# Kernel tuning notes

Measured on AMD Instinct MI355X. Metric: run time of the kernel, lower is better.

Reference implementation:

```python
import jax, jax.numpy as jnp
import numpy as np

K = 3
PAD = 1


def _conv_offset(x, w_off, b_off):
    # standard 3x3 conv, stride 1, pad 1, with bias -> [B, 18, H, W]
    y = jax.lax.conv_general_dilated(
        x, w_off, window_strides=(1, 1), padding=((PAD, PAD), (PAD, PAD)),
        dimension_numbers=('NCHW', 'OIHW', 'NCHW'))
    return y + b_off[None, :, None, None]


def _deform_conv(x, offset, w_dcn):
    # x: [B,Cin,H,W], offset: [B,2*K*K,H,W] (dy,dx interleaved per tap), w_dcn: [Cout,Cin,K,K]
    B, Cin, H, W = x.shape
    KK = K * K
    Ho, Wo = offset.shape[2], offset.shape[3]

    ky = jnp.repeat(jnp.arange(K), K)          # [KK] kernel row index
    kx = jnp.tile(jnp.arange(K), K)            # [KK] kernel col index
    off = offset.reshape(B, KK, 2, Ho, Wo)
    dy, dx = off[:, :, 0], off[:, :, 1]        # [B,KK,Ho,Wo]

    gy = (jnp.arange(Ho)[None, :, None] - PAD + ky[:, None, None]).astype(x.dtype)  # [KK,Ho,1]
    gx = (jnp.arange(Wo)[None, None, :] - PAD + kx[:, None, None]).astype(x.dtype)  # [KK,1,Wo]
    py = gy[None] + dy                         # [B,KK,Ho,Wo] sampling rows
    px = gx[None] + dx                         # [B,KK,Ho,Wo] sampling cols

    y0 = jnp.floor(py); x0 = jnp.floor(px)
    wy1 = py - y0; wx1 = px - x0
    wy0 = 1.0 - wy1; wx0 = 1.0 - wx1

    x_flat = x.reshape(B, Cin, H * W)

    def gather(yi, xi, wgt):
        valid = (yi >= 0) & (yi <= H - 1) & (xi >= 0) & (xi <= W - 1)
        yc = jnp.clip(yi, 0, H - 1).astype(jnp.int32)
        xc = jnp.clip(xi, 0, W - 1).astype(jnp.int32)
        idx = yc * W + xc                      # [B,KK,Ho,Wo]
        vals = jax.vmap(lambda xb, ib: xb[:, ib])(x_flat, idx)  # [B,Cin,KK,Ho,Wo]
        w = (wgt * valid.astype(x.dtype))[:, None]              # [B,1,KK,Ho,Wo]
        return vals * w

    sampled = (gather(y0, x0, wy0 * wx0)
               + gather(y0, x0 + 1, wy0 * wx1)
               + gather(y0 + 1, x0, wy1 * wx0)
               + gather(y0 + 1, x0 + 1, wy1 * wx1))  # [B,Cin,KK,Ho,Wo]

    wr = w_dcn.reshape(w_dcn.shape[0], Cin, KK)
    return jnp.einsum('bckhw,ock->bohw', sampled, wr)


def setup_inputs() -> dict:
    key = jax.random.key(0)
    k1, k2, k3, k4 = jax.random.split(key, 4)
    B, Cin, H, W = 8, 32, 160, 160
    Cout = 32
    x = jax.random.normal(k1, (B, Cin, H, W), jnp.float32)
    w_off = jax.random.normal(k2, (2 * K * K, Cin, K, K), jnp.float32) * 0.01
    b_off = jax.random.normal(k3, (2 * K * K,), jnp.float32) * 0.01
    w_dcn = jax.random.normal(k4, (Cout, Cin, K, K), jnp.float32) * 0.1
    return {'x': x, 'w_off': w_off, 'b_off': b_off, 'w_dcn': w_dcn}


def reference(x, w_off, b_off, w_dcn):
    offset = _conv_offset(x, w_off, b_off)
    y = _deform_conv(x, offset, w_dcn)
    return jax.nn.relu(y)
```

## Files before the change

### kernel.cpp

```cpp
#include <hip/hip_runtime.h>

#define H_ 160
#define W_ 160
#define HW_ (H_ * W_)
#define NPIX (8 * HW_)


typedef __attribute__((ext_vector_type(8)))  short  short8;
typedef __attribute__((ext_vector_type(4)))  float  f32x4;
typedef __attribute__((ext_vector_type(2)))  float  f32x2;
typedef __attribute__((ext_vector_type(16))) float  f32x16;
typedef __attribute__((ext_vector_type(4)))  unsigned u32x4;

__device__ __forceinline__ unsigned short bf16_rne(float f) {
    unsigned u = __float_as_uint(f);
    u += 0x7fffu + ((u >> 16) & 1u);
    return (unsigned short)(u >> 16);
}
__device__ __forceinline__ unsigned pack2_bf16(float a, float b) {
    unsigned ua = __float_as_uint(a); ua += 0x7fffu + ((ua >> 16) & 1u);
    unsigned ub = __float_as_uint(b); ub += 0x7fffu + ((ub >> 16) & 1u);
    return (ua >> 16) | (ub & 0xffff0000u);
}
__device__ __forceinline__ f32x2 up2(unsigned u) {
    f32x2 r;
    r.x = __uint_as_float(u << 16);
    r.y = __uint_as_float(u & 0xffff0000u);
    return r;
}

__global__ __launch_bounds__(256) void nhwc_bf16(
    const float* __restrict__ x, unsigned short* __restrict__ xT)
{
    const int pix = blockIdx.x * 256 + threadIdx.x;
    const int p = pix % HW_;
    const int b = pix / HW_;
    const float* __restrict__ src = x + (size_t)b * 32 * HW_ + p;
    unsigned* __restrict__ dst = (unsigned*)(xT + (size_t)pix * 32);
    #pragma unroll
    for (int g = 0; g < 16; ++g)
        dst[g] = pack2_bf16(src[(2 * g) * HW_], src[(2 * g + 1) * HW_]);
}

__global__ __launch_bounds__(256, 5) void dcn_fused(
    const unsigned short* __restrict__ xT,
    const float* __restrict__ w_off,
    const float* __restrict__ b_off,
    const float* __restrict__ w_dcn,
    float* __restrict__ out)
{
    __shared__ __align__(16) unsigned short wsh[9 * 2 * 64 * 8];
    __shared__ float offl[4 * 18 * 33];
    __shared__ float bl[32];
    const int tid = threadIdx.x;

    for (int d = tid; d < 9 * 1024; d += 256) {
        const int tap = d >> 10, r = d & 1023, j = r >> 5, c = r & 31;
        const int s = c >> 4, kg = (c >> 3) & 1;
        const int unit = (tap * 2 + s) * 64 + j + 32 * kg;
        wsh[unit * 8 + (c & 7)] = (j < 18) ? bf16_rne(w_off[(j * 32 + c) * 9 + tap])
                                           : (unsigned short)0;
    }
    if (tid < 32) bl[tid] = (tid < 18) ? b_off[tid] : 0.0f;
    __syncthreads();

    const int wave = tid >> 6, lane = tid & 63;
    const int n = lane & 31;
    const int hh = lane >> 5;
    const int pixbase = blockIdx.x * 128 + wave * 32;
    const int pix = pixbase + n;
    const int w = pix % W_, h = (pix / W_) % H_, b = pix / HW_;
    const unsigned short* __restrict__ xb = xT + (size_t)b * HW_ * 32 + hh * 8;

    {
        f32x16 acc = {};
        const u32x4 z4 = {0u, 0u, 0u, 0u};
        #pragma unroll
        for (int tap = 0; tap < 9; ++tap) {
            const int yy = h - 1 + tap / 3;
            const int xx = w - 1 + tap % 3;
            const bool valid = (yy >= 0) && (yy < H_) && (xx >= 0) && (xx < W_);
            const int idx = min(max(yy, 0), H_ - 1) * W_ + min(max(xx, 0), W_ - 1);
            const unsigned short* __restrict__ px_ = xb + (size_t)idx * 32;
            u32x4 l0 = *(const u32x4*)(px_);
            u32x4 l1 = *(const u32x4*)(px_ + 16);
            l0 = valid ? l0 : z4;
            l1 = valid ? l1 : z4;
            const short8 a0 = __builtin_bit_cast(short8, l0);
            const short8 a1 = __builtin_bit_cast(short8, l1);
            const short8 b0 = *(const short8*)(wsh + ((tap * 2 + 0) * 64 + lane) * 8);
            const short8 b1 = *(const short8*)(wsh + ((tap * 2 + 1) * 64 + lane) * 8);
            acc = __builtin_amdgcn_mfma_f32_32x32x16_bf16(a0, b0, acc, 0, 0, 0);
            acc = __builtin_amdgcn_mfma_f32_32x32x16_bf16(a1, b1, acc, 0, 0, 0);
        }
        float* __restrict__ owp = offl + wave * 594;
        if (n < 18) {
            const float bia = bl[n];
            #pragma unroll
            for (int r = 0; r < 16; ++r) {
                const int prow = (r & 3) + 8 * (r >> 2) + 4 * hh;
                owp[n * 33 + prow] = acc[r] + bia;
            }
        }
    }
    __syncthreads();

    for (int d = tid; d < 9 * 1024; d += 256) {
        const int tap = d >> 10, r = d & 1023, j = r >> 5, c = r & 31;
        const int s = c >> 4, kg = (c >> 3) & 1;
        const int unit = (tap * 2 + s) * 64 + j + 32 * kg;
        wsh[unit * 8 + (c & 7)] = bf16_rne(w_dcn[(j * 32 + c) * 9 + tap]);
    }
    __syncthreads();

    const float* __restrict__ ow = offl + wave * 594;
    f32x16 acc = {};

    #pragma unroll
    for (int tap = 0; tap < 9; ++tap) {
        const float dy = ow[(2 * tap) * 33 + n];
        const float dx = ow[(2 * tap + 1) * 33 + n];
        const float py = (float)(h - 1 + tap / 3) + dy;
        const float px = (float)(w - 1 + tap % 3) + dx;
        const float fy0 = floorf(py), fx0 = floorf(px);
        const float wy1 = py - fy0, wx1 = px - fx0;
        const float wy0 = 1.0f - wy1, wx0 = 1.0f - wx1;
        const int y0 = (int)fy0, x0 = (int)fx0;
        const bool vy0 = (y0 >= 0) && (y0 < H_);
        const bool vy1 = (y0 + 1 >= 0) && (y0 + 1 < H_);
        const bool vx0 = (x0 >= 0) && (x0 < W_);
        const bool vx1 = (x0 + 1 >= 0) && (x0 + 1 < W_);
        const float w00 = (vy0 && vx0) ? wy0 * wx0 : 0.0f;
        const float w01 = (vy0 && vx1) ? wy0 * wx1 : 0.0f;
        const float w10 = (vy1 && vx0) ? wy1 * wx0 : 0.0f;
        const float w11 = (vy1 && vx1) ? wy1 * wx1 : 0.0f;
        const int yc0 = min(max(y0, 0), H_ - 1), yc1 = min(max(y0 + 1, 0), H_ - 1);
        const int xc0 = min(max(x0, 0), W_ - 1), xc1 = min(max(x0 + 1, 0), W_ - 1);

        const unsigned short* __restrict__ pA = xb + (size_t)(yc0 * W_ + xc0) * 32;
        const unsigned short* __restrict__ pB = xb + (size_t)(yc0 * W_ + xc1) * 32;
        const unsigned short* __restrict__ pC = xb + (size_t)(yc1 * W_ + xc0) * 32;
        const unsigned short* __restrict__ pD = xb + (size_t)(yc1 * W_ + xc1) * 32;
        const u32x4 A0 = *(const u32x4*)(pA);      const u32x4 A1 = *(const u32x4*)(pA + 16);
        const u32x4 B0 = *(const u32x4*)(pB);      const u32x4 B1 = *(const u32x4*)(pB + 16);
        const u32x4 C0 = *(const u32x4*)(pC);      const u32x4 C1 = *(const u32x4*)(pC + 16);
        const u32x4 D0 = *(const u32x4*)(pD);      const u32x4 D1 = *(const u32x4*)(pD + 16);

        #define COMB(a, bb, cc, dd) ({ \
            const f32x2 v = up2(a) * w00 + up2(bb) * w01 + up2(cc) * w10 + up2(dd) * w11; \
            pack2_bf16(v.x, v.y); })
        u32x4 av0, av1;
        av0.x = COMB(A0.x, B0.x, C0.x, D0.x);
        av0.y = COMB(A0.y, B0.y, C0.y, D0.y);
        av0.z = COMB(A0.z, B0.z, C0.z, D0.z);
        av0.w = COMB(A0.w, B0.w, C0.w, D0.w);
        av1.x = COMB(A1.x, B1.x, C1.x, D1.x);
        av1.y = COMB(A1.y, B1.y, C1.y, D1.y);
        av1.z = COMB(A1.z, B1.z, C1.z, D1.z);
        av1.w = COMB(A1.w, B1.w, C1.w, D1.w);
        #undef COMB

        const short8 a0 = __builtin_bit_cast(short8, av0);
        const short8 a1 = __builtin_bit_cast(short8, av1);
        const short8 b0 = *(const short8*)(wsh + ((tap * 2 + 0) * 64 + lane) * 8);
        const short8 b1 = *(const short8*)(wsh + ((tap * 2 + 1) * 64 + lane) * 8);
        acc = __builtin_amdgcn_mfma_f32_32x32x16_bf16(a0, b0, acc, 0, 0, 0);
        acc = __builtin_amdgcn_mfma_f32_32x32x16_bf16(a1, b1, acc, 0, 0, 0);
    }

    float* __restrict__ ob = out + (size_t)b * 32 * HW_ + (size_t)n * HW_
                           + (pixbase - b * HW_) + 4 * hh;
    #pragma unroll
    for (int g = 0; g < 4; ++g) {
        f32x4 r;
        #pragma unroll
        for (int i = 0; i < 4; ++i) r[i] = fmaxf(acc[g * 4 + i], 0.0f);
        *(f32x4*)(ob + g * 8) = r;
    }
}

extern "C" void kernel_launch(void* const* d_in, const int* in_sizes, int n_in,
                              void* d_out, int out_size, void* d_ws, size_t ws_size,
                              hipStream_t stream) {
    const float* x     = (const float*)d_in[0];
    const float* w_off = (const float*)d_in[1];
    const float* b_off = (const float*)d_in[2];
    const float* w_dcn = (const float*)d_in[3];
    float* out = (float*)d_out;

    unsigned short* xT = (unsigned short*)d_ws;

    nhwc_bf16<<<800, 256, 0, stream>>>(x, xT);
    dcn_fused<<<1600, 256, 0, stream>>>(xT, w_off, b_off, w_dcn, out);
}
```

Measured before the change: 153.7 us.

## Software-pipeline bilinear gathers across taps and remap block order per XCD

The deform-conv tap loop now issues the four corner gathers for the next tap before combining and running the MFMAs for the current one. This double-buffers the loaded values in registers so global-load latency overlaps compute. Block indices are remapped so that consecutive hardware block IDs, which are dispatched round-robin across the 8 XCDs, each map to a contiguous range of pixels, which should improve L2 locality. The launch-bounds occupancy hint drops from 5 to 4 blocks per CU, allowing more registers for the extra buffers at the cost of fewer resident waves.

```diff
diff --git a/kernel.cpp b/kernel.cpp
--- a/kernel.cpp
+++ b/kernel.cpp
@@ -42,7 +42,7 @@
         dst[g] = pack2_bf16(src[(2 * g) * HW_], src[(2 * g + 1) * HW_]);
 }
 
-__global__ __launch_bounds__(256, 5) void dcn_fused(
+__global__ __launch_bounds__(256, 4) void dcn_fused(
     const unsigned short* __restrict__ xT,
     const float* __restrict__ w_off,
     const float* __restrict__ b_off,
@@ -67,7 +67,8 @@
     const int wave = tid >> 6, lane = tid & 63;
     const int n = lane & 31;
     const int hh = lane >> 5;
-    const int pixbase = blockIdx.x * 128 + wave * 32;
+    const int bid = (blockIdx.x & 7) * 200 + (blockIdx.x >> 3);
+    const int pixbase = bid * 128 + wave * 32;
     const int pix = pixbase + n;
     const int w = pix % W_, h = (pix / W_) % H_, b = pix / HW_;
     const unsigned short* __restrict__ xb = xT + (size_t)b * HW_ * 32 + hh * 8;
@@ -116,48 +117,58 @@
     const float* __restrict__ ow = offl + wave * 594;
     f32x16 acc = {};
 
+    u32x4 gA0[2], gA1[2], gB0[2], gB1[2], gC0[2], gC1[2], gD0[2], gD1[2];
+    f32x4 cw[2];
+
+    #define PREP(t, s) do { \
+        const float dy = ow[(2 * (t)) * 33 + n]; \
+        const float dx = ow[(2 * (t) + 1) * 33 + n]; \
+        const float py = (float)(h - 1 + (t) / 3) + dy; \
+        const float px = (float)(w - 1 + (t) % 3) + dx; \
+        const float fy0 = floorf(py), fx0 = floorf(px); \
+        const float wy1 = py - fy0, wx1 = px - fx0; \
+        const float wy0 = 1.0f - wy1, wx0 = 1.0f - wx1; \
+        const int y0 = (int)fy0, x0 = (int)fx0; \
+        const bool vy0 = (y0 >= 0) && (y0 < H_); \
+        const bool vy1 = (y0 + 1 >= 0) && (y0 + 1 < H_); \
+        const bool vx0 = (x0 >= 0) && (x0 < W_); \
+        const bool vx1 = (x0 + 1 >= 0) && (x0 + 1 < W_); \
+        cw[s].x = (vy0 && vx0) ? wy0 * wx0 : 0.0f; \
+        cw[s].y = (vy0 && vx1) ? wy0 * wx1 : 0.0f; \
+        cw[s].z = (vy1 && vx0) ? wy1 * wx0 : 0.0f; \
+        cw[s].w = (vy1 && vx1) ? wy1 * wx1 : 0.0f; \
+        const int yc0 = min(max(y0, 0), H_ - 1), yc1 = min(max(y0 + 1, 0), H_ - 1); \
+        const int xc0 = min(max(x0, 0), W_ - 1), xc1 = min(max(x0 + 1, 0), W_ - 1); \
+        const unsigned short* pA = xb + (size_t)(yc0 * W_ + xc0) * 32; \
+        const unsigned short* pB = xb + (size_t)(yc0 * W_ + xc1) * 32; \
+        const unsigned short* pC = xb + (size_t)(yc1 * W_ + xc0) * 32; \
+        const unsigned short* pD = xb + (size_t)(yc1 * W_ + xc1) * 32; \
+        gA0[s] = *(const u32x4*)(pA);  gA1[s] = *(const u32x4*)(pA + 16); \
+        gB0[s] = *(const u32x4*)(pB);  gB1[s] = *(const u32x4*)(pB + 16); \
+        gC0[s] = *(const u32x4*)(pC);  gC1[s] = *(const u32x4*)(pC + 16); \
+        gD0[s] = *(const u32x4*)(pD);  gD1[s] = *(const u32x4*)(pD + 16); \
+    } while (0)
+
+    PREP(0, 0);
     #pragma unroll
     for (int tap = 0; tap < 9; ++tap) {
-        const float dy = ow[(2 * tap) * 33 + n];
-        const float dx = ow[(2 * tap + 1) * 33 + n];
-        const float py = (float)(h - 1 + tap / 3) + dy;
-        const float px = (float)(w - 1 + tap % 3) + dx;
-        const float fy0 = floorf(py), fx0 = floorf(px);
-        const float wy1 = py - fy0, wx1 = px - fx0;
-        const float wy0 = 1.0f - wy1, wx0 = 1.0f - wx1;
-        const int y0 = (int)fy0, x0 = (int)fx0;
-        const bool vy0 = (y0 >= 0) && (y0 < H_);
-        const bool vy1 = (y0 + 1 >= 0) && (y0 + 1 < H_);
-        const bool vx0 = (x0 >= 0) && (x0 < W_);
-        const bool vx1 = (x0 + 1 >= 0) && (x0 + 1 < W_);
-        const float w00 = (vy0 && vx0) ? wy0 * wx0 : 0.0f;
-        const float w01 = (vy0 && vx1) ? wy0 * wx1 : 0.0f;
-        const float w10 = (vy1 && vx0) ? wy1 * wx0 : 0.0f;
-        const float w11 = (vy1 && vx1) ? wy1 * wx1 : 0.0f;
-        const int yc0 = min(max(y0, 0), H_ - 1), yc1 = min(max(y0 + 1, 0), H_ - 1);
-        const int xc0 = min(max(x0, 0), W_ - 1), xc1 = min(max(x0 + 1, 0), W_ - 1);
-
-        const unsigned short* __restrict__ pA = xb + (size_t)(yc0 * W_ + xc0) * 32;
-        const unsigned short* __restrict__ pB = xb + (size_t)(yc0 * W_ + xc1) * 32;
-        const unsigned short* __restrict__ pC = xb + (size_t)(yc1 * W_ + xc0) * 32;
-        const unsigned short* __restrict__ pD = xb + (size_t)(yc1 * W_ + xc1) * 32;
-        const u32x4 A0 = *(const u32x4*)(pA);      const u32x4 A1 = *(const u32x4*)(pA + 16);
-        const u32x4 B0 = *(const u32x4*)(pB);      const u32x4 B1 = *(const u32x4*)(pB + 16);
-        const u32x4 C0 = *(const u32x4*)(pC);      const u32x4 C1 = *(const u32x4*)(pC + 16);
-        const u32x4 D0 = *(const u32x4*)(pD);      const u32x4 D1 = *(const u32x4*)(pD + 16);
-
+        const int cur = tap & 1, nxt = cur ^ 1;
+        if (tap < 8) PREP(tap + 1, nxt);
+
+        const float w00 = cw[cur].x, w01 = cw[cur].y;
+        const float w10 = cw[cur].z, w11 = cw[cur].w;
         #define COMB(a, bb, cc, dd) ({ \
             const f32x2 v = up2(a) * w00 + up2(bb) * w01 + up2(cc) * w10 + up2(dd) * w11; \
             pack2_bf16(v.x, v.y); })
         u32x4 av0, av1;
-        av0.x = COMB(A0.x, B0.x, C0.x, D0.x);
-        av0.y = COMB(A0.y, B0.y, C0.y, D0.y);
-        av0.z = COMB(A0.z, B0.z, C0.z, D0.z);
-        av0.w = COMB(A0.w, B0.w, C0.w, D0.w);
-        av1.x = COMB(A1.x, B1.x, C1.x, D1.x);
-        av1.y = COMB(A1.y, B1.y, C1.y, D1.y);
-        av1.z = COMB(A1.z, B1.z, C1.z, D1.z);
-        av1.w = COMB(A1.w, B1.w, C1.w, D1.w);
+        av0.x = COMB(gA0[cur].x, gB0[cur].x, gC0[cur].x, gD0[cur].x);
+        av0.y = COMB(gA0[cur].y, gB0[cur].y, gC0[cur].y, gD0[cur].y);
+        av0.z = COMB(gA0[cur].z, gB0[cur].z, gC0[cur].z, gD0[cur].z);
+        av0.w = COMB(gA0[cur].w, gB0[cur].w, gC0[cur].w, gD0[cur].w);
+        av1.x = COMB(gA1[cur].x, gB1[cur].x, gC1[cur].x, gD1[cur].x);
+        av1.y = COMB(gA1[cur].y, gB1[cur].y, gC1[cur].y, gD1[cur].y);
+        av1.z = COMB(gA1[cur].z, gB1[cur].z, gC1[cur].z, gD1[cur].z);
+        av1.w = COMB(gA1[cur].w, gB1[cur].w, gC1[cur].w, gD1[cur].w);
         #undef COMB
 
         const short8 a0 = __builtin_bit_cast(short8, av0);
@@ -167,6 +178,7 @@
         acc = __builtin_amdgcn_mfma_f32_32x32x16_bf16(a0, b0, acc, 0, 0, 0);
         acc = __builtin_amdgcn_mfma_f32_32x32x16_bf16(a1, b1, acc, 0, 0, 0);
     }
+    #undef PREP
 
     float* __restrict__ ob = out + (size_t)b * 32 * HW_ + (size_t)n * HW_
                            + (pixbase - b * HW_) + 4 * hh;
```

Result: faster. 148.0 us (-3.8%).
